# Optimization experiments

Hardware: AMD Instinct MI355X
Metric: run time of the kernel (lower is better)

## Reference

```python
import jax, jax.numpy as jnp
import numpy as np

DDD = (0.83, 0.68, 0.54, 0.41, 0.29, 0.18, 0.09, 0.0)  # SONNET decile thresholds
NUM_INSTANCES = 16  # fixed label budget: mask values in 0..NUM_INSTANCES (0 = background)


def setup_inputs() -> dict:
    key = jax.random.key(0)
    k1, k2, k3 = jax.random.split(key, 3)
    B, C, W, H = 2, 8, 128, 128
    pred = jax.random.normal(k1, (B, C, W, H), dtype=jnp.float32)
    mask = jax.random.randint(k2, (B, W, H), 0, NUM_INSTANCES + 1, dtype=jnp.int32)
    ignored_map = jax.random.uniform(k3, (B, W, H), dtype=jnp.float32)
    return {"pred": pred, "mask": mask, "ignored_map": ignored_map}


def _edt(nuclei):
    """Exact Euclidean distance transform of boolean masks, vectorized over [B,K].
    nuclei: bool [B,K,W,H]. Returns float32 [B,K,W,H]: distance from each True
    pixel to the nearest False pixel (0 on False pixels), matching
    scipy.ndimage.distance_transform_edt via the separable squared-EDT identity
    D2[i,j] = min_{j'} ( G2[i,j'] + (j-j')^2 ),  G2[i,j] = min_{i': bg[i',j]} (i-i')^2.
    """
    bg = ~nuclei
    B, K, W, H = nuclei.shape
    INF = jnp.float32(1e9)
    di = jnp.arange(W, dtype=jnp.float32)
    d2i = (di[:, None] - di[None, :]) ** 2  # [W, W'] squared row offsets
    # G2[b,k,i,j] = min over i' (background rows) of (i - i')^2   -> [B,K,W,H]
    G2 = jnp.min(jnp.where(bg[:, :, None, :, :], d2i[None, None, :, :, None], INF), axis=3)
    dj = jnp.arange(H, dtype=jnp.float32)
    d2j = (dj[:, None] - dj[None, :]) ** 2  # [H, H'] squared column offsets
    # D2[b,k,i,j] = min over j' of G2[b,k,i,j'] + (j - j')^2
    D2 = jnp.min(G2[:, :, :, None, :] + d2j[None, None, None, :, :], axis=4)
    return jnp.sqrt(D2)


def _build_gt_sonnet(mask):
    """mask: int [B,W,H] instance labels (0 = background) -> gt_sonnet float32 [B,8,W,H]."""
    labels = jnp.arange(1, NUM_INSTANCES + 1, dtype=mask.dtype)
    nuclei = mask[:, None, :, :] == labels[None, :, None, None]  # [B,K,W,H]
    d = _edt(nuclei)
    # per-instance normalization: norm(img) = img / max(img) if max != 0
    m = jnp.max(d, axis=(2, 3), keepdims=True)
    d = jnp.where(m > 0, d / jnp.where(m > 0, m, 1.0), d)
    # thresholding: <0.5 -> 0, then >0.7 -> 1
    d = jnp.where(d < 0.5, 0.0, d)
    d = jnp.where(d > 0.7, 1.0, d)
    ddd = jnp.asarray(DDD, dtype=jnp.float32)  # [8] lower bin edges
    hi = jnp.concatenate([jnp.asarray([jnp.inf], dtype=jnp.float32), ddd[:-1]])  # upper edges (i==0 unbounded)
    de = d[:, :, None, :, :]  # [B,K,1,W,H]
    bins = (de >= ddd[None, None, :, None, None]) & (de < hi[None, None, :, None, None])
    # restricting to nuclei matches the original for all bins (bin 0 needs d>=0.83>0,
    # and background pixels have d==0, so they never enter bin 0 anyway)
    bins = bins & nuclei[:, :, None, :, :]
    return jnp.sum(bins.astype(jnp.float32), axis=1)  # [B,8,W,H]


def reference(pred, mask, ignored_map):
    gt_sonnet = _build_gt_sonnet(mask)
    diff = pred - gt_sonnet
    ad = jnp.abs(diff)
    l1 = jnp.where(ad < 1.0, 0.5 * diff * diff, ad - 0.5)  # SmoothL1, beta=1
    offset_loss = jnp.mean(jnp.mean(l1, axis=1) * ignored_map)
    return offset_loss, gt_sonnet
```

## Files before the change

kernel.cpp:

```cpp
#include <hip/hip_runtime.h>

#define KK 16
#define NPIX 16384


__global__ __launch_bounds__(256) void edt_kernel(const int* __restrict__ mask,
                                                  int* __restrict__ maxpart,
                                                  float* __restrict__ acc,
                                                  unsigned int* __restrict__ cnt,
                                                  unsigned short* __restrict__ d2) {
    __shared__ unsigned char  nuc[NPIX];
    __shared__ unsigned short sdn[NPIX];
    __shared__ unsigned short sup[NPIX];
    __shared__ int wmax[4];

    const int bid = blockIdx.x;
    const int t   = threadIdx.x;
    const int b1  = bid >> 7;
    const int k1  = (bid >> 3) & 15;
    const int rg  = bid & 7;

    if (bid == 0 && t == 0) { *acc = 0.0f; *cnt = 0u; }

    const int label = k1 + 1;
    const int4* m4 = (const int4*)(mask + b1 * NPIX);
    #pragma unroll
    for (int it = 0; it < 16; ++it) {
        const int idx = t + 256 * it;
        const int4 v = m4[idx];
        uchar4 u;
        u.x = (v.x == label); u.y = (v.y == label);
        u.z = (v.z == label); u.w = (v.w == label);
        *(uchar4*)&nuc[idx * 4] = u;
    }
    __syncthreads();

    if (t < 128) {
        const int j = t;
        int dist = 200;
        for (int i = 0; i < 128; ++i) {
            dist = nuc[i * 128 + j] ? min(dist + 1, 200) : 0;
            sdn[i * 128 + j] = (unsigned short)dist;
        }
    } else {
        const int j = t - 128;
        int dist = 200;
        for (int i = 127; i >= 0; --i) {
            dist = nuc[i * 128 + j] ? min(dist + 1, 200) : 0;
            sup[i * 128 + j] = (unsigned short)dist;
        }
    }
    __syncthreads();

    #pragma unroll
    for (int it = 0; it < 64; ++it) {
        const int idx = t + 256 * it;
        const int nd = min((int)sdn[idx], (int)sup[idx]);
        sdn[idx] = (unsigned short)(nd * nd);
    }
    __syncthreads();

    const int row = rg * 16 + (t >> 4);
    const int c0  = (t & 15) * 8;
    const unsigned short* grow = &sdn[row * 128];
    int best[8];
    #pragma unroll
    for (int u = 0; u < 8; ++u) best[u] = 0x7fffffff;
    for (int jp = 0; jp < 128; ++jp) {
        const int g = (int)grow[jp];
        #pragma unroll
        for (int u = 0; u < 8; ++u) {
            const int dj = c0 + u - jp;
            best[u] = min(best[u], g + dj * dj);
        }
    }

    uint4 w;
    w.x = (unsigned)best[0] | ((unsigned)best[1] << 16);
    w.y = (unsigned)best[2] | ((unsigned)best[3] << 16);
    w.z = (unsigned)best[4] | ((unsigned)best[5] << 16);
    w.w = (unsigned)best[6] | ((unsigned)best[7] << 16);
    *(uint4*)(d2 + (b1 * KK + k1) * NPIX + row * 128 + c0) = w;

    int bm = 0;
    #pragma unroll
    for (int u = 0; u < 8; ++u) bm = max(bm, best[u]);
    #pragma unroll
    for (int off = 32; off; off >>= 1) bm = max(bm, __shfl_down(bm, off, 64));
    if ((t & 63) == 0) wmax[t >> 6] = bm;
    __syncthreads();
    if (t == 0)
        maxpart[bid] = max(max(wmax[0], wmax[1]), max(wmax[2], wmax[3]));
}

__global__ __launch_bounds__(256) void gt_loss_kernel(const float* __restrict__ pred,
                                                      const float* __restrict__ ign,
                                                      const int* __restrict__ mask,
                                                      const unsigned short* __restrict__ d2,
                                                      const int* __restrict__ maxpart,
                                                      float* __restrict__ out,
                                                      float* __restrict__ acc,
                                                      unsigned int* __restrict__ cnt) {
    __shared__ float msq[KK];
    __shared__ float wred[4];

    const int bid = blockIdx.x;
    const int t   = threadIdx.x;
    const int p   = bid * 256 + t;
    const int b   = bid >> 6;
    const int pp  = p & (NPIX - 1);

    if (t < KK) {
        const int base = b * 128 + t * 8;
        int mt = 0;
        #pragma unroll
        for (int r = 0; r < 8; ++r) mt = max(mt, maxpart[base + r]);
        msq[t] = __fsqrt_rn((float)mt);
    }
    __syncthreads();

    const int label = mask[p];
    int cbin = -1;
    if (label > 0) {
        const int k = label - 1;
        const float d  = __fsqrt_rn((float)d2[(b * KK + k) * NPIX + pp]);
        float dn = __fdiv_rn(d, msq[k]);
        if (dn < 0.5f) dn = 0.0f;
        if (dn > 0.7f) dn = 1.0f;
        const float ddd[8] = {0.83f, 0.68f, 0.54f, 0.41f, 0.29f, 0.18f, 0.09f, 0.0f};
        #pragma unroll
        for (int c = 0; c < 8; ++c) {
            if (cbin < 0 && dn >= ddd[c]) cbin = c;
        }
    }

    float lsum = 0.0f;
    #pragma unroll
    for (int c = 0; c < 8; ++c) {
        const float g = (c == cbin) ? 1.0f : 0.0f;
        out[1 + (b * 8 + c) * NPIX + pp] = g;
        const float diff = pred[(b * 8 + c) * NPIX + pp] - g;
        const float ad = fabsf(diff);
        lsum += (ad < 1.0f) ? 0.5f * diff * diff : (ad - 0.5f);
    }
    float contrib = lsum * 0.125f * ign[p];

    #pragma unroll
    for (int off = 32; off; off >>= 1) contrib += __shfl_down(contrib, off, 64);
    if ((t & 63) == 0) wred[t >> 6] = contrib;
    __syncthreads();

    if (t == 0) {
        atomicAdd(acc, (wred[0] + wred[1]) + (wred[2] + wred[3]));
        __threadfence();
        const unsigned int old = atomicAdd(cnt, 1u);
        if (old == 127u) {
            const float total = atomicAdd(acc, 0.0f);
            out[0] = total * (1.0f / 32768.0f);
        }
    }
}

extern "C" void kernel_launch(void* const* d_in, const int* in_sizes, int n_in,
                              void* d_out, int out_size, void* d_ws, size_t ws_size,
                              hipStream_t stream) {
    const float* pred = (const float*)d_in[0];
    const int*   mask = (const int*)d_in[1];
    const float* ign  = (const float*)d_in[2];
    float* out = (float*)d_out;

    int*            maxpart = (int*)d_ws;
    float*          acc     = (float*)((char*)d_ws + 1024);
    unsigned int*   cnt     = (unsigned int*)((char*)d_ws + 1028);
    unsigned short* d2      = (unsigned short*)((char*)d_ws + 4096);

    edt_kernel<<<256, 256, 0, stream>>>(mask, maxpart, acc, cnt, d2);
    gt_loss_kernel<<<128, 256, 0, stream>>>(pred, ign, mask, d2, maxpart, out, acc, cnt);
}
```

Measured before the change: 78.58 us.

## Prune row EDT min-search with expanding window and early exit

Replaces the full 128-column scan in the second EDT pass with a search that starts from the thread's own 8 columns and expands outward. It stops once the squared offset exceeds every current best in the wavefront, which is an exact pruning. The column scan loops gain unroll pragmas, and the loss kernel is relaunched as 256 blocks of 128 threads, with the block count check updated to match. The expanding loop adds divergence and wave-wide vote overhead, and with sparse random masks most distances are small, so it should terminate early.

```diff
diff --git a/kernel.cpp b/kernel.cpp
--- a/kernel.cpp
+++ b/kernel.cpp
@@ -9,9 +9,9 @@
                                                   float* __restrict__ acc,
                                                   unsigned int* __restrict__ cnt,
                                                   unsigned short* __restrict__ d2) {
-    __shared__ unsigned char  nuc[NPIX];
-    __shared__ unsigned short sdn[NPIX];
-    __shared__ unsigned short sup[NPIX];
+    __shared__ alignas(16) unsigned char  nuc[NPIX];
+    __shared__ alignas(16) unsigned short sdn[NPIX];
+    __shared__ alignas(16) unsigned short sup[NPIX];
     __shared__ int wmax[4];
 
     const int bid = blockIdx.x;
@@ -38,6 +38,7 @@
     if (t < 128) {
         const int j = t;
         int dist = 200;
+        #pragma unroll 4
         for (int i = 0; i < 128; ++i) {
             dist = nuc[i * 128 + j] ? min(dist + 1, 200) : 0;
             sdn[i * 128 + j] = (unsigned short)dist;
@@ -45,6 +46,7 @@
     } else {
         const int j = t - 128;
         int dist = 200;
+        #pragma unroll 4
         for (int i = 127; i >= 0; --i) {
             dist = nuc[i * 128 + j] ? min(dist + 1, 200) : 0;
             sup[i * 128 + j] = (unsigned short)dist;
@@ -63,16 +65,52 @@
     const int row = rg * 16 + (t >> 4);
     const int c0  = (t & 15) * 8;
     const unsigned short* grow = &sdn[row * 128];
+
+    const uint4 gv = *(const uint4*)(grow + c0);
+    int g[8];
+    g[0] = (int)(gv.x & 0xffffu); g[1] = (int)(gv.x >> 16);
+    g[2] = (int)(gv.y & 0xffffu); g[3] = (int)(gv.y >> 16);
+    g[4] = (int)(gv.z & 0xffffu); g[5] = (int)(gv.z >> 16);
+    g[6] = (int)(gv.w & 0xffffu); g[7] = (int)(gv.w >> 16);
+
     int best[8];
     #pragma unroll
     for (int u = 0; u < 8; ++u) best[u] = 0x7fffffff;
-    for (int jp = 0; jp < 128; ++jp) {
-        const int g = (int)grow[jp];
+    #pragma unroll
+    for (int w = 0; w < 8; ++w) {
         #pragma unroll
         for (int u = 0; u < 8; ++u) {
-            const int dj = c0 + u - jp;
-            best[u] = min(best[u], g + dj * dj);
-        }
+            const int dj = u - w;
+            best[u] = min(best[u], g[w] + dj * dj);
+        }
+    }
+    int mb = 0;
+    #pragma unroll
+    for (int u = 0; u < 8; ++u) mb = max(mb, best[u]);
+
+    for (int e = 0; e < 128; ++e) {
+        if (!__any((e + 1) * (e + 1) < mb)) break;
+        const int jl = c0 - 1 - e;
+        const int jr = c0 + 8 + e;
+        if (jl >= 0) {
+            const int gl = (int)grow[jl];
+            #pragma unroll
+            for (int u = 0; u < 8; ++u) {
+                const int dj = u + 1 + e;
+                best[u] = min(best[u], gl + dj * dj);
+            }
+        }
+        if (jr < 128) {
+            const int gr = (int)grow[jr];
+            #pragma unroll
+            for (int u = 0; u < 8; ++u) {
+                const int dj = 8 + e - u;
+                best[u] = min(best[u], gr + dj * dj);
+            }
+        }
+        mb = 0;
+        #pragma unroll
+        for (int u = 0; u < 8; ++u) mb = max(mb, best[u]);
     }
 
     uint4 w;
@@ -82,9 +120,7 @@
     w.w = (unsigned)best[6] | ((unsigned)best[7] << 16);
     *(uint4*)(d2 + (b1 * KK + k1) * NPIX + row * 128 + c0) = w;
 
-    int bm = 0;
-    #pragma unroll
-    for (int u = 0; u < 8; ++u) bm = max(bm, best[u]);
+    int bm = mb;
     #pragma unroll
     for (int off = 32; off; off >>= 1) bm = max(bm, __shfl_down(bm, off, 64));
     if ((t & 63) == 0) wmax[t >> 6] = bm;
@@ -93,7 +129,7 @@
         maxpart[bid] = max(max(wmax[0], wmax[1]), max(wmax[2], wmax[3]));
 }
 
-__global__ __launch_bounds__(256) void gt_loss_kernel(const float* __restrict__ pred,
+__global__ __launch_bounds__(128) void gt_loss_kernel(const float* __restrict__ pred,
                                                       const float* __restrict__ ign,
                                                       const int* __restrict__ mask,
                                                       const unsigned short* __restrict__ d2,
@@ -102,12 +138,12 @@
                                                       float* __restrict__ acc,
                                                       unsigned int* __restrict__ cnt) {
     __shared__ float msq[KK];
-    __shared__ float wred[4];
+    __shared__ float wred[2];
 
     const int bid = blockIdx.x;
     const int t   = threadIdx.x;
-    const int p   = bid * 256 + t;
-    const int b   = bid >> 6;
+    const int p   = bid * 128 + t;
+    const int b   = bid >> 7;
     const int pp  = p & (NPIX - 1);
 
     if (t < KK) {
@@ -151,10 +187,10 @@
     __syncthreads();
 
     if (t == 0) {
-        atomicAdd(acc, (wred[0] + wred[1]) + (wred[2] + wred[3]));
+        atomicAdd(acc, wred[0] + wred[1]);
         __threadfence();
         const unsigned int old = atomicAdd(cnt, 1u);
-        if (old == 127u) {
+        if (old == 255u) {
             const float total = atomicAdd(acc, 0.0f);
             out[0] = total * (1.0f / 32768.0f);
         }
@@ -175,5 +211,5 @@
     unsigned short* d2      = (unsigned short*)((char*)d_ws + 4096);
 
     edt_kernel<<<256, 256, 0, stream>>>(mask, maxpart, acc, cnt, d2);
-    gt_loss_kernel<<<128, 256, 0, stream>>>(pred, ign, mask, d2, maxpart, out, acc, cnt);
+    gt_loss_kernel<<<256, 128, 0, stream>>>(pred, ign, mask, d2, maxpart, out, acc, cnt);
 }
```

Result: faster. 75.09 us (-4.4%).

## Compute per-pixel own-label EDT via expanding ring search instead of full per-instance EDT

Applied to the files above, without the earlier changes.

Replaces the dense per-instance separable EDT (16 labels × full image) with a single pass computing, for each pixel, the squared distance to the nearest pixel of a different label using an expanding Chebyshev ring search with early wave-wide termination. Per-label maxima are gathered via shared atomics into a per-row partial table, and the loss kernel reduces these. This removes the O(W·H·K·W) work and the large intermediate buffer. The cost is data-dependent: large uniform regions would make the ring search slow.

```diff
diff --git a/kernel.cpp b/kernel.cpp
--- a/kernel.cpp
+++ b/kernel.cpp
@@ -4,127 +4,123 @@
 #define NPIX 16384
 
 
-__global__ __launch_bounds__(256) void edt_kernel(const int* __restrict__ mask,
-                                                  int* __restrict__ maxpart,
-                                                  float* __restrict__ acc,
-                                                  unsigned int* __restrict__ cnt,
-                                                  unsigned short* __restrict__ d2) {
-    __shared__ unsigned char  nuc[NPIX];
-    __shared__ unsigned short sdn[NPIX];
-    __shared__ unsigned short sup[NPIX];
-    __shared__ int wmax[4];
+__global__ __launch_bounds__(128) void edt_own_kernel(const int* __restrict__ mask,
+                                                      int* __restrict__ maxpart,
+                                                      float* __restrict__ acc,
+                                                      unsigned int* __restrict__ cnt,
+                                                      unsigned short* __restrict__ d2own) {
+    __shared__ int lab[3][128];
+    __shared__ int lmax[KK];
 
     const int bid = blockIdx.x;
     const int t   = threadIdx.x;
-    const int b1  = bid >> 7;
-    const int k1  = (bid >> 3) & 15;
-    const int rg  = bid & 7;
+    const int b   = bid >> 7;
+    const int r   = bid & 127;
 
     if (bid == 0 && t == 0) { *acc = 0.0f; *cnt = 0u; }
+    if (t < KK) lmax[t] = 0;
 
-    const int label = k1 + 1;
-    const int4* m4 = (const int4*)(mask + b1 * NPIX);
-    #pragma unroll
-    for (int it = 0; it < 16; ++it) {
-        const int idx = t + 256 * it;
-        const int4 v = m4[idx];
-        uchar4 u;
-        u.x = (v.x == label); u.y = (v.y == label);
-        u.z = (v.z == label); u.w = (v.w == label);
-        *(uchar4*)&nuc[idx * 4] = u;
-    }
+    const int* mrow = mask + b * NPIX + r * 128;
+    lab[1][t] = mrow[t];
+    lab[0][t] = (r > 0)   ? mrow[t - 128] : 255;
+    lab[2][t] = (r < 127) ? mrow[t + 128] : 255;
     __syncthreads();
 
-    if (t < 128) {
-        const int j = t;
-        int dist = 200;
-        for (int i = 0; i < 128; ++i) {
-            dist = nuc[i * 128 + j] ? min(dist + 1, 200) : 0;
-            sdn[i * 128 + j] = (unsigned short)dist;
-        }
+    const int l = lab[1][t];
+    int best;
+    if (l == 0) {
+        best = 0;
     } else {
-        const int j = t - 128;
-        int dist = 200;
-        for (int i = 127; i >= 0; --i) {
-            dist = nuc[i * 128 + j] ? min(dist + 1, 200) : 0;
-            sup[i * 128 + j] = (unsigned short)dist;
-        }
+        best = 0x7fffffff;
+        const int lf = (t > 0)   ? lab[1][t - 1] : l;
+        const int rt = (t < 127) ? lab[1][t + 1] : l;
+        if (lf != l) best = 1;
+        if (rt != l) best = 1;
+        const int up = lab[0][t];
+        const int dn = lab[2][t];
+        if (up != l && up != 255) best = min(best, 1);
+        if (dn != l && dn != 255) best = min(best, 1);
+        const int ul = (t > 0)   ? lab[0][t - 1] : 255;
+        const int ur = (t < 127) ? lab[0][t + 1] : 255;
+        const int dl = (t > 0)   ? lab[2][t - 1] : 255;
+        const int dr = (t < 127) ? lab[2][t + 1] : 255;
+        if (ul != l && ul != 255) best = min(best, 2);
+        if (ur != l && ur != 255) best = min(best, 2);
+        if (dl != l && dl != 255) best = min(best, 2);
+        if (dr != l && dr != 255) best = min(best, 2);
     }
-    __syncthreads();
 
-    #pragma unroll
-    for (int it = 0; it < 64; ++it) {
-        const int idx = t + 256 * it;
-        const int nd = min((int)sdn[idx], (int)sup[idx]);
-        sdn[idx] = (unsigned short)(nd * nd);
-    }
-    __syncthreads();
-
-    const int row = rg * 16 + (t >> 4);
-    const int c0  = (t & 15) * 8;
-    const unsigned short* grow = &sdn[row * 128];
-    int best[8];
-    #pragma unroll
-    for (int u = 0; u < 8; ++u) best[u] = 0x7fffffff;
-    for (int jp = 0; jp < 128; ++jp) {
-        const int g = (int)grow[jp];
-        #pragma unroll
-        for (int u = 0; u < 8; ++u) {
-            const int dj = c0 + u - jp;
-            best[u] = min(best[u], g + dj * dj);
+    for (int e = 2; e < 128; ++e) {
+        if (!__any(e * e < best)) break;
+        if (e * e < best) {
+            const int* mimg = mask + b * NPIX;
+            for (int di = -e; di <= e; ++di) {
+                const int rr = r + di;
+                if (rr < 0 || rr > 127) continue;
+                const int* rw = mimg + rr * 128;
+                const int ad = (di < 0) ? -di : di;
+                if (ad == e) {
+                    const int j0 = max(t - e, 0), j1 = min(t + e, 127);
+                    for (int jj = j0; jj <= j1; ++jj) {
+                        if (rw[jj] != l) {
+                            const int dj = jj - t;
+                            best = min(best, di * di + dj * dj);
+                        }
+                    }
+                } else {
+                    const int jl = t - e, jr = t + e;
+                    if (jl >= 0  && rw[jl] != l) best = min(best, di * di + e * e);
+                    if (jr <= 127 && rw[jr] != l) best = min(best, di * di + e * e);
+                }
+            }
         }
     }
 
-    uint4 w;
-    w.x = (unsigned)best[0] | ((unsigned)best[1] << 16);
-    w.y = (unsigned)best[2] | ((unsigned)best[3] << 16);
-    w.z = (unsigned)best[4] | ((unsigned)best[5] << 16);
-    w.w = (unsigned)best[6] | ((unsigned)best[7] << 16);
-    *(uint4*)(d2 + (b1 * KK + k1) * NPIX + row * 128 + c0) = w;
+    best = min(best, 40000);
+    d2own[b * NPIX + r * 128 + t] = (unsigned short)best;
 
-    int bm = 0;
-    #pragma unroll
-    for (int u = 0; u < 8; ++u) bm = max(bm, best[u]);
-    #pragma unroll
-    for (int off = 32; off; off >>= 1) bm = max(bm, __shfl_down(bm, off, 64));
-    if ((t & 63) == 0) wmax[t >> 6] = bm;
+    if (l > 0) atomicMax(&lmax[l - 1], best);
     __syncthreads();
-    if (t == 0)
-        maxpart[bid] = max(max(wmax[0], wmax[1]), max(wmax[2], wmax[3]));
+    if (t < KK) maxpart[bid * KK + t] = lmax[t];
 }
 
-__global__ __launch_bounds__(256) void gt_loss_kernel(const float* __restrict__ pred,
+__global__ __launch_bounds__(128) void gt_loss_kernel(const float* __restrict__ pred,
                                                       const float* __restrict__ ign,
                                                       const int* __restrict__ mask,
-                                                      const unsigned short* __restrict__ d2,
+                                                      const unsigned short* __restrict__ d2own,
                                                       const int* __restrict__ maxpart,
                                                       float* __restrict__ out,
                                                       float* __restrict__ acc,
                                                       unsigned int* __restrict__ cnt) {
+    __shared__ int   lmax2[KK];
     __shared__ float msq[KK];
-    __shared__ float wred[4];
+    __shared__ float wred[2];
 
     const int bid = blockIdx.x;
     const int t   = threadIdx.x;
-    const int p   = bid * 256 + t;
-    const int b   = bid >> 6;
+    const int p   = bid * 128 + t;
+    const int b   = bid >> 7;
     const int pp  = p & (NPIX - 1);
 
-    if (t < KK) {
-        const int base = b * 128 + t * 8;
-        int mt = 0;
+    if (t < KK) lmax2[t] = 0;
+    __syncthreads();
+    {
+        const int k = t & 15, c = t >> 4;
+        const int* mp = maxpart + b * (128 * KK) + c * (16 * KK) + k;
+        int pm = 0;
         #pragma unroll
-        for (int r = 0; r < 8; ++r) mt = max(mt, maxpart[base + r]);
-        msq[t] = __fsqrt_rn((float)mt);
+        for (int rr = 0; rr < 16; ++rr) pm = max(pm, mp[rr * KK]);
+        atomicMax(&lmax2[k], pm);
     }
+    __syncthreads();
+    if (t < KK) msq[t] = __fsqrt_rn((float)lmax2[t]);
     __syncthreads();
 
     const int label = mask[p];
     int cbin = -1;
     if (label > 0) {
-        const int k = label - 1;
-        const float d  = __fsqrt_rn((float)d2[(b * KK + k) * NPIX + pp]);
-        float dn = __fdiv_rn(d, msq[k]);
+        const float d  = __fsqrt_rn((float)d2own[p]);
+        float dn = __fdiv_rn(d, msq[label - 1]);
         if (dn < 0.5f) dn = 0.0f;
         if (dn > 0.7f) dn = 1.0f;
         const float ddd[8] = {0.83f, 0.68f, 0.54f, 0.41f, 0.29f, 0.18f, 0.09f, 0.0f};
@@ -151,10 +147,10 @@
     __syncthreads();
 
     if (t == 0) {
-        atomicAdd(acc, (wred[0] + wred[1]) + (wred[2] + wred[3]));
+        atomicAdd(acc, wred[0] + wred[1]);
         __threadfence();
         const unsigned int old = atomicAdd(cnt, 1u);
-        if (old == 127u) {
+        if (old == 255u) {
             const float total = atomicAdd(acc, 0.0f);
             out[0] = total * (1.0f / 32768.0f);
         }
@@ -170,10 +166,10 @@
     float* out = (float*)d_out;
 
     int*            maxpart = (int*)d_ws;
-    float*          acc     = (float*)((char*)d_ws + 1024);
-    unsigned int*   cnt     = (unsigned int*)((char*)d_ws + 1028);
-    unsigned short* d2      = (unsigned short*)((char*)d_ws + 4096);
+    float*          acc     = (float*)((char*)d_ws + 16384);
+    unsigned int*   cnt     = (unsigned int*)((char*)d_ws + 16388);
+    unsigned short* d2own   = (unsigned short*)((char*)d_ws + 20480);
 
-    edt_kernel<<<256, 256, 0, stream>>>(mask, maxpart, acc, cnt, d2);
-    gt_loss_kernel<<<128, 256, 0, stream>>>(pred, ign, mask, d2, maxpart, out, acc, cnt);
+    edt_own_kernel<<<256, 128, 0, stream>>>(mask, maxpart, acc, cnt, d2own);
+    gt_loss_kernel<<<256, 128, 0, stream>>>(pred, ign, mask, d2own, maxpart, out, acc, cnt);
 }
```

Result: faster. 70.14 us (-10.7%).
